# Optimization experiments

Measured on AMD Instinct MI355X. Metric: run time of the kernel, lower is better.

Reference implementation:

```python
import jax, jax.numpy as jnp
import numpy as np

HEAD = 8
EMB = 512
D_K = EMB // HEAD


def setup_inputs() -> dict:
    key = jax.random.key(0)
    ks = jax.random.split(key, 12)
    B, S = 2, 2048
    scale = 1.0 / np.sqrt(EMB)
    inp = {
        "query": jax.random.normal(ks[0], (B, S, EMB), jnp.float32),
        "key": jax.random.normal(ks[1], (B, S, EMB), jnp.float32),
        "value": jax.random.normal(ks[2], (B, S, EMB), jnp.float32),
        # subsequentMask(size): lower-triangular causal mask, shape [1, S, S]
        "mask": jnp.tril(jnp.ones((1, S, S), jnp.int32)),
        "Wq": jax.random.normal(ks[3], (EMB, EMB), jnp.float32) * scale,
        "bq": jnp.zeros((EMB,), jnp.float32),
        "Wk": jax.random.normal(ks[4], (EMB, EMB), jnp.float32) * scale,
        "bk": jnp.zeros((EMB,), jnp.float32),
        "Wv": jax.random.normal(ks[5], (EMB, EMB), jnp.float32) * scale,
        "bv": jnp.zeros((EMB,), jnp.float32),
        "Wo": jax.random.normal(ks[6], (EMB, EMB), jnp.float32) * scale,
        "bo": jnp.zeros((EMB,), jnp.float32),
    }
    return inp


def _split_heads(x, B):
    # [B, S, E] -> [B, H, S, d_k]
    return x.reshape(B, -1, HEAD, D_K).transpose(0, 2, 1, 3)


def reference(query, key, value, mask, Wq, bq, Wk, bk, Wv, bv, Wo, bo):
    B, S, _ = query.shape
    # linear projections (x @ W^T + b, torch nn.Linear convention)
    q = _split_heads(query @ Wq.T + bq, B)
    k = _split_heads(key @ Wk.T + bk, B)
    v = _split_heads(value @ Wv.T + bv, B)
    # scaled dot-product attention; scores [B, H, S, S]
    scores = jnp.einsum('bhqd,bhkd->bhqk', q, k) / jnp.sqrt(jnp.float32(D_K))
    # mask [1,S,S] -> unsqueeze(0) -> [1,1,S,S]; masked_fill(mask==0, -1e9)
    m = mask[None, ...]  # [1, 1, S, S]
    scores = jnp.where(m == 0, jnp.float32(-1e9), scores)
    p_attn = jax.nn.softmax(scores, axis=-1)
    # dropout is identity at inference (deterministic reference)
    x = jnp.einsum('bhqk,bhkd->bhqd', p_attn, v)
    x = x.transpose(0, 2, 1, 3).reshape(B, S, EMB)
    return x @ Wo.T + bo
```

## Files before the change

### kernel.cpp

```cpp
#include <hip/hip_runtime.h>
#include <hip/hip_bf16.h>


#define SEQ 2048
#define EMB 512
#define NH  8
#define DKD 64

typedef __bf16 bf16x8 __attribute__((ext_vector_type(8)));
typedef ushort u16x8  __attribute__((ext_vector_type(8)));
typedef float  f32x4  __attribute__((ext_vector_type(4)));

__device__ __forceinline__ ushort f2bf(float f) {
  unsigned x = __float_as_uint(f);
  return (ushort)((x + 0x7fffu + ((x >> 16) & 1u)) >> 16);
}
__device__ __forceinline__ unsigned pkbf(float a, float b) {
  __hip_bfloat162 h = __float22bfloat162_rn(make_float2(a, b));
  unsigned u;
  __builtin_memcpy(&u, &h, 4);
  return u;
}

__device__ __forceinline__ void cp16(const ushort* g, ushort* l) {
  __builtin_amdgcn_global_load_lds(
      (const __attribute__((address_space(1))) void*)g,
      (__attribute__((address_space(3))) void*)l, 16, 0, 0);
}

__global__ __launch_bounds__(256) void cvt7(
    const float* s0, const float* s1, const float* s2, const float* s3,
    const float* s4, const float* s5, const float* s6,
    ushort* d0, ushort* d1, ushort* d2, ushort* d3,
    ushort* d4, ushort* d5, ushort* d6) {
  const float* src; ushort* dst; int n;
  switch (blockIdx.y) {
    case 0: src = s0; dst = d0; n = 2 * SEQ * EMB; break;
    case 1: src = s1; dst = d1; n = 2 * SEQ * EMB; break;
    case 2: src = s2; dst = d2; n = 2 * SEQ * EMB; break;
    case 3: src = s3; dst = d3; n = EMB * EMB;     break;
    case 4: src = s4; dst = d4; n = EMB * EMB;     break;
    case 5: src = s5; dst = d5; n = EMB * EMB;     break;
    default: src = s6; dst = d6; n = EMB * EMB;    break;
  }
  int i = (blockIdx.x * 256 + threadIdx.x) * 8;
  if (i >= n) return;
  float4 a = *reinterpret_cast<const float4*>(src + i);
  float4 b = *reinterpret_cast<const float4*>(src + i + 4);
  uint4 t = make_uint4(pkbf(a.x, a.y), pkbf(a.z, a.w),
                       pkbf(b.x, b.y), pkbf(b.z, b.w));
  *reinterpret_cast<uint4*>(dst + i) = t;
}

__device__ __forceinline__ void gemm_body(const ushort* __restrict__ X,
                                          const ushort* __restrict__ W,
                                          const float* __restrict__ bias,
                                          void* __restrict__ C,
                                          int mode, bool of32, float oscale,
                                          ushort* sA, ushort* sB) {
  const int N = EMB, K = EMB;
  const int tid = threadIdx.x;
  const int w = tid >> 6, lane = tid & 63, r16 = lane & 15, g = lane >> 4;
  const int nT = N / 64;
  const int m0 = (blockIdx.x / nT) * 128;
  const int n0 = (blockIdx.x % nT) * 64;
  const int wm = w * 32;

  f32x4 acc[2][4] = {};

  auto stage = [&](int buf, int k0) {
#pragma unroll
    for (int i = 0; i < 2; ++i) {
      const int s = i * 256 + w * 64 + lane;
      const int row = s >> 2;
      const int col = (s & 3) ^ ((row >> 1) & 3);
      cp16(X + (size_t)(m0 + row) * K + k0 + col * 8, sA + buf * 4096 + s * 8);
    }
    {
      const int s = w * 64 + lane;
      const int row = s >> 2;
      const int col = (s & 3) ^ ((row >> 1) & 3);
      cp16(W + (size_t)(n0 + row) * K + k0 + col * 8, sB + buf * 2048 + s * 8);
    }
  };

  stage(0, 0);
  const int NIT = K / 32;
  for (int it = 0; it < NIT; ++it) {
    const int cur = it & 1;
    __syncthreads();
    if (it + 1 < NIT) stage(cur ^ 1, (it + 1) * 32);

    const ushort* bA = sA + cur * 4096;
    const ushort* bB = sB + cur * 2048;
    bf16x8 af[2], bfr[4];
#pragma unroll
    for (int f = 0; f < 2; ++f) {
      const int row = wm + f * 16 + r16;
      af[f] = *reinterpret_cast<const bf16x8*>(bA + row * 32 + ((g ^ ((row >> 1) & 3)) << 3));
    }
#pragma unroll
    for (int t = 0; t < 4; ++t) {
      const int row = t * 16 + r16;
      bfr[t] = *reinterpret_cast<const bf16x8*>(bB + row * 32 + ((g ^ ((row >> 1) & 3)) << 3));
    }
#pragma unroll
    for (int f = 0; f < 2; ++f)
#pragma unroll
      for (int t = 0; t < 4; ++t)
        acc[f][t] = __builtin_amdgcn_mfma_f32_16x16x32_bf16(af[f], bfr[t], acc[f][t], 0, 0, 0);
  }

#pragma unroll
  for (int t = 0; t < 4; ++t) {
    const int n = n0 + t * 16 + r16;
    const float bv = bias[n];
#pragma unroll
    for (int f = 0; f < 2; ++f) {
#pragma unroll
      for (int r = 0; r < 4; ++r) {
        const int m = m0 + wm + f * 16 + g * 4 + r;
        const float v = (acc[f][t][r] + bv) * oscale;
        size_t addr;
        if (mode == 0) {
          addr = (size_t)m * N + n;
        } else {
          const int b = m >> 11, s = m & (SEQ - 1);
          const int h = n >> 6, dk = n & (DKD - 1);
          addr = (mode == 1) ? (((size_t)(b * NH + h) * SEQ + s) * DKD + dk)
                             : (((size_t)(b * NH + h) * DKD + dk) * SEQ + s);
        }
        if (of32) ((float*)C)[addr] = v;
        else      ((ushort*)C)[addr] = f2bf(v);
      }
    }
  }
}

__global__ __launch_bounds__(256) void proj_qkv(
    const ushort* Xq, const ushort* Xk, const ushort* Xv,
    const ushort* Wq, const ushort* Wk, const ushort* Wv,
    const float* bq, const float* bk, const float* bv,
    ushort* Qo, ushort* Ko, ushort* Vo) {
  __shared__ __align__(16) ushort sA[2 * 128 * 32];
  __shared__ __align__(16) ushort sB[2 * 64 * 32];
  const int z = blockIdx.z;
  const ushort* X = (z == 0) ? Xq : (z == 1) ? Xk : Xv;
  const ushort* W = (z == 0) ? Wq : (z == 1) ? Wk : Wv;
  const float* bias = (z == 0) ? bq : (z == 1) ? bk : bv;
  ushort* C = (z == 0) ? Qo : (z == 1) ? Ko : Vo;
  gemm_body(X, W, bias, C, (z == 2) ? 2 : 1, false,
            (z == 0) ? 0.18033688011112042f : 1.0f, sA, sB);
}

__global__ __launch_bounds__(256) void out_proj(const ushort* X, const ushort* W,
                                                const float* bias, float* C) {
  __shared__ __align__(16) ushort sA[2 * 128 * 32];
  __shared__ __align__(16) ushort sB[2 * 64 * 32];
  gemm_body(X, W, bias, C, 0, true, 1.0f, sA, sB);
}

__global__ __launch_bounds__(256) void flash_attn(const ushort* __restrict__ Q,
                                                  const ushort* __restrict__ Kb,
                                                  const ushort* __restrict__ Vt,
                                                  ushort* __restrict__ O) {
  __shared__ __align__(16) ushort sK[2][64 * 64];
  __shared__ __align__(16) ushort sV[2][64 * 64];
  __shared__ __align__(16) ushort sP[4][16 * 64];

  const int tid = threadIdx.x, w = tid >> 6, lane = tid & 63;
  const int r16 = lane & 15, g = lane >> 4;
  const int bh = blockIdx.x & 15;
  const int j  = blockIdx.x >> 4;
  const int qb = (j < 16) ? (31 - j) : (j - 16);
  const int q0 = qb * 64 + w * 16;
  const int q  = q0 + r16;

  const ushort* qp = Q + ((size_t)bh * SEQ + q0 + r16) * DKD + g * 8;
  const bf16x8 qf0 = *reinterpret_cast<const bf16x8*>(qp);
  const bf16x8 qf1 = *reinterpret_cast<const bf16x8*>(qp + 32);

  f32x4 oacc[4] = {};
  float psum = 0.f;

  const ushort* kbase = Kb + (size_t)bh * SEQ * DKD;
  const ushort* vbase = Vt + (size_t)bh * DKD * SEQ;

  auto stageKV = [&](int buf, int kb) {
#pragma unroll
    for (int i = 0; i < 2; ++i) {
      const int s = i * 256 + w * 64 + lane;
      const int row = s >> 3;
      const int col = (s & 7) ^ (row & 7);
      cp16(kbase + (size_t)(kb + row) * DKD + col * 8, &sK[buf][(size_t)(i * 256 + w * 64) * 8]);
      cp16(vbase + (size_t)row * SEQ + kb + col * 8,   &sV[buf][(size_t)(i * 256 + w * 64) * 8]);
    }
  };

  stageKV(0, 0);
  const int ntiles = qb + 1;
  for (int kt = 0; kt < ntiles; ++kt) {
    const int cur = kt & 1;
    const int kb = kt * 64;
    __syncthreads();
    if (kt + 1 < ntiles) stageKV(cur ^ 1, (kt + 1) * 64);

    f32x4 sc[4] = {};
#pragma unroll
    for (int t = 0; t < 4; ++t) {
      const int row = t * 16 + r16;
      const bf16x8 a0 = *reinterpret_cast<const bf16x8*>(&sK[cur][row * 64 + (((0 + g) ^ (row & 7)) << 3)]);
      const bf16x8 a1 = *reinterpret_cast<const bf16x8*>(&sK[cur][row * 64 + (((4 + g) ^ (row & 7)) << 3)]);
      sc[t] = __builtin_amdgcn_mfma_f32_16x16x32_bf16(a0, qf0, sc[t], 0, 0, 0);
      sc[t] = __builtin_amdgcn_mfma_f32_16x16x32_bf16(a1, qf1, sc[t], 0, 0, 0);
    }

    const bool diag = (kb + 63) > q0;
    float p[16];
#pragma unroll
    for (int t = 0; t < 4; ++t)
#pragma unroll
      for (int r = 0; r < 4; ++r) {
        float e = __builtin_amdgcn_exp2f(sc[t][r]);
        if (diag && (kb + t * 16 + g * 4 + r) > q) e = 0.f;
        p[t * 4 + r] = e;
      }
    float s0 = (p[0] + p[1]) + (p[2] + p[3]);
    float s1 = (p[4] + p[5]) + (p[6] + p[7]);
    float s2 = (p[8] + p[9]) + (p[10] + p[11]);
    float s3 = (p[12] + p[13]) + (p[14] + p[15]);
    psum += (s0 + s1) + (s2 + s3);

#pragma unroll
    for (int t = 0; t < 4; ++t) {
      const unsigned lo = pkbf(p[t * 4],     p[t * 4 + 1]);
      const unsigned hi = pkbf(p[t * 4 + 2], p[t * 4 + 3]);
      const int key0 = t * 16 + g * 4;
      const int slot = (key0 >> 3) ^ (r16 & 7);
      *reinterpret_cast<uint2*>(&sP[w][r16 * 64 + slot * 8 + (key0 & 7)]) = make_uint2(lo, hi);
    }
    __asm__ volatile("s_waitcnt lgkmcnt(0)" ::: "memory");

    const bf16x8 pf0 = *reinterpret_cast<const bf16x8*>(&sP[w][r16 * 64 + (((0 + g) ^ (r16 & 7)) << 3)]);
    const bf16x8 pf1 = *reinterpret_cast<const bf16x8*>(&sP[w][r16 * 64 + (((4 + g) ^ (r16 & 7)) << 3)]);
#pragma unroll
    for (int t = 0; t < 4; ++t) {
      const int row = t * 16 + r16;
      const bf16x8 b0 = *reinterpret_cast<const bf16x8*>(&sV[cur][row * 64 + (((0 + g) ^ (row & 7)) << 3)]);
      const bf16x8 b1 = *reinterpret_cast<const bf16x8*>(&sV[cur][row * 64 + (((4 + g) ^ (row & 7)) << 3)]);
      oacc[t] = __builtin_amdgcn_mfma_f32_16x16x32_bf16(pf0, b0, oacc[t], 0, 0, 0);
      oacc[t] = __builtin_amdgcn_mfma_f32_16x16x32_bf16(pf1, b1, oacc[t], 0, 0, 0);
    }
  }

  psum += __shfl_xor(psum, 16);
  psum += __shfl_xor(psum, 32);
  const float inv = 1.0f / psum;
  const int b = bh >> 3, h = bh & 7;
#pragma unroll
  for (int r = 0; r < 4; ++r) {
    const float ir = __shfl(inv, g * 4 + r);
    const int mq = q0 + g * 4 + r;
#pragma unroll
    for (int t = 0; t < 4; ++t)
      O[((size_t)b * SEQ + mq) * EMB + h * DKD + t * 16 + r16] = f2bf(oacc[t][r] * ir);
  }
}

extern "C" void kernel_launch(void* const* d_in, const int* in_sizes, int n_in,
                              void* d_out, int out_size, void* d_ws, size_t ws_size,
                              hipStream_t stream) {
  const float* q_in = (const float*)d_in[0];
  const float* k_in = (const float*)d_in[1];
  const float* v_in = (const float*)d_in[2];
  const float* Wq = (const float*)d_in[4];
  const float* bq = (const float*)d_in[5];
  const float* Wk = (const float*)d_in[6];
  const float* bk = (const float*)d_in[7];
  const float* Wv = (const float*)d_in[8];
  const float* bv = (const float*)d_in[9];
  const float* Wo = (const float*)d_in[10];
  const float* bo = (const float*)d_in[11];
  float* out = (float*)d_out;
  ushort* ws = (ushort*)d_ws;

  const size_t NX = (size_t)2 * SEQ * EMB;
  const size_t NW = (size_t)EMB * EMB;
  ushort* Xq = ws;
  ushort* Xk = Xq + NX;
  ushort* Xv = Xk + NX;
  ushort* WqB = Xv + NX;
  ushort* WkB = WqB + NW;
  ushort* WvB = WkB + NW;
  ushort* WoB = WvB + NW;
  ushort* Qb  = WoB + NW;
  ushort* Kbf = Qb + NX;
  ushort* Vbf = Kbf + NX;
  ushort* Ab  = Vbf + NX;

  dim3 blk(256);
  cvt7<<<dim3(1024, 7), blk, 0, stream>>>(q_in, k_in, v_in, Wq, Wk, Wv, Wo,
                                          Xq, Xk, Xv, WqB, WkB, WvB, WoB);
  proj_qkv<<<dim3((2 * SEQ / 128) * (EMB / 64), 1, 3), blk, 0, stream>>>(
      Xq, Xk, Xv, WqB, WkB, WvB, bq, bk, bv, Qb, Kbf, Vbf);
  flash_attn<<<dim3(16 * (SEQ / 64)), blk, 0, stream>>>(Qb, Kbf, Vbf, Ab);
  out_proj<<<dim3((2 * SEQ / 128) * (EMB / 64)), blk, 0, stream>>>(Ab, WoB, bo, out);
}
```

Measured before the change: 174.0 us.

## Split causal attention KV range across two blocks and merge partials

Each query block's KV tiles are split into two halves processed by separate workgroups, doubling the flash attention grid. Each half writes unnormalized fp32 partial outputs and row sums to workspace. A new attn_norm kernel adds the two partials, normalizes, converts to bf16 and writes the head-interleaved layout. This targets causal load imbalance and low block count, at the cost of extra fp32 global traffic and one more launch.

```diff
diff --git a/kernel.cpp b/kernel.cpp
--- a/kernel.cpp
+++ b/kernel.cpp
@@ -163,16 +163,27 @@
 __global__ __launch_bounds__(256) void flash_attn(const ushort* __restrict__ Q,
                                                   const ushort* __restrict__ Kb,
                                                   const ushort* __restrict__ Vt,
-                                                  ushort* __restrict__ O) {
+                                                  float* __restrict__ O0,
+                                                  float* __restrict__ O1,
+                                                  float* __restrict__ P0,
+                                                  float* __restrict__ P1) {
   __shared__ __align__(16) ushort sK[2][64 * 64];
   __shared__ __align__(16) ushort sV[2][64 * 64];
   __shared__ __align__(16) ushort sP[4][16 * 64];
 
   const int tid = threadIdx.x, w = tid >> 6, lane = tid & 63;
   const int r16 = lane & 15, g = lane >> 4;
-  const int bh = blockIdx.x & 15;
-  const int j  = blockIdx.x >> 4;
-  const int qb = (j < 16) ? (31 - j) : (j - 16);
+  const int g2 = blockIdx.x & 3;
+  const int c  = blockIdx.x >> 2;
+  const int bh = c & 15;
+  const int t4 = c >> 4;
+  const int qb = (g2 < 2) ? (31 - t4) : t4;
+  const int half = g2 & 1;
+  const int tiles = qb + 1;
+  const int hs  = (tiles + 1) >> 1;
+  const int kt0 = half ? hs : 0;
+  const int kt1 = half ? tiles : hs;
+
   const int q0 = qb * 64 + w * 16;
   const int q  = q0 + r16;
 
@@ -197,13 +208,12 @@
     }
   };
 
-  stageKV(0, 0);
-  const int ntiles = qb + 1;
-  for (int kt = 0; kt < ntiles; ++kt) {
-    const int cur = kt & 1;
+  if (kt0 < kt1) stageKV(0, kt0 * 64);
+  for (int kt = kt0; kt < kt1; ++kt) {
+    const int cur = (kt - kt0) & 1;
     const int kb = kt * 64;
     __syncthreads();
-    if (kt + 1 < ntiles) stageKV(cur ^ 1, (kt + 1) * 64);
+    if (kt + 1 < kt1) stageKV(cur ^ 1, (kt + 1) * 64);
 
     f32x4 sc[4] = {};
 #pragma unroll
@@ -255,16 +265,40 @@
 
   psum += __shfl_xor(psum, 16);
   psum += __shfl_xor(psum, 32);
-  const float inv = 1.0f / psum;
+  float* Pc = half ? P1 : P0;
+  float* Oc = half ? O1 : O0;
+  if (g == 0) Pc[(size_t)bh * SEQ + q0 + r16] = psum;
+#pragma unroll
+  for (int r = 0; r < 4; ++r) {
+    const int mq = q0 + g * 4 + r;
+#pragma unroll
+    for (int t = 0; t < 4; ++t)
+      Oc[((size_t)bh * SEQ + mq) * DKD + t * 16 + r16] = oacc[t][r];
+  }
+}
+
+__global__ __launch_bounds__(256) void attn_norm(const float* __restrict__ O0,
+                                                 const float* __restrict__ O1,
+                                                 const float* __restrict__ P0,
+                                                 const float* __restrict__ P1,
+                                                 ushort* __restrict__ Ab) {
+  const int idx = blockIdx.x * 256 + threadIdx.x;
+  const int d0 = (idx & 7) * 8;
+  const int s  = (idx >> 3) & (SEQ - 1);
+  const int bh = idx >> 14;
+  const size_t o = ((size_t)bh * SEQ + s) * DKD + d0;
+  const float4 a0 = *reinterpret_cast<const float4*>(O0 + o);
+  const float4 a1 = *reinterpret_cast<const float4*>(O0 + o + 4);
+  const float4 b0 = *reinterpret_cast<const float4*>(O1 + o);
+  const float4 b1 = *reinterpret_cast<const float4*>(O1 + o + 4);
+  const float inv = 1.0f / (P0[(size_t)bh * SEQ + s] + P1[(size_t)bh * SEQ + s]);
+  uint4 t = make_uint4(
+      pkbf((a0.x + b0.x) * inv, (a0.y + b0.y) * inv),
+      pkbf((a0.z + b0.z) * inv, (a0.w + b0.w) * inv),
+      pkbf((a1.x + b1.x) * inv, (a1.y + b1.y) * inv),
+      pkbf((a1.z + b1.z) * inv, (a1.w + b1.w) * inv));
   const int b = bh >> 3, h = bh & 7;
-#pragma unroll
-  for (int r = 0; r < 4; ++r) {
-    const float ir = __shfl(inv, g * 4 + r);
-    const int mq = q0 + g * 4 + r;
-#pragma unroll
-    for (int t = 0; t < 4; ++t)
-      O[((size_t)b * SEQ + mq) * EMB + h * DKD + t * 16 + r16] = f2bf(oacc[t][r] * ir);
-  }
+  *reinterpret_cast<uint4*>(Ab + ((size_t)b * SEQ + s) * EMB + h * DKD + d0) = t;
 }
 
 extern "C" void kernel_launch(void* const* d_in, const int* in_sizes, int n_in,
@@ -297,12 +331,17 @@
   ushort* Kbf = Qb + NX;
   ushort* Vbf = Kbf + NX;
   ushort* Ab  = Vbf + NX;
+  float*  O0  = (float*)(Ab + NX);
+  float*  O1  = O0 + (size_t)2 * NH * SEQ * DKD;
+  float*  P0  = O1 + (size_t)2 * NH * SEQ * DKD;
+  float*  P1  = P0 + (size_t)2 * NH * SEQ;
 
   dim3 blk(256);
   cvt7<<<dim3(1024, 7), blk, 0, stream>>>(q_in, k_in, v_in, Wq, Wk, Wv, Wo,
                                           Xq, Xk, Xv, WqB, WkB, WvB, WoB);
   proj_qkv<<<dim3((2 * SEQ / 128) * (EMB / 64), 1, 3), blk, 0, stream>>>(
       Xq, Xk, Xv, WqB, WkB, WvB, bq, bk, bv, Qb, Kbf, Vbf);
-  flash_attn<<<dim3(16 * (SEQ / 64)), blk, 0, stream>>>(Qb, Kbf, Vbf, Ab);
+  flash_attn<<<dim3(16 * 32 * 2), blk, 0, stream>>>(Qb, Kbf, Vbf, O0, O1, P0, P1);
+  attn_norm<<<dim3(1024), blk, 0, stream>>>(O0, O1, P0, P1, Ab);
   out_proj<<<dim3((2 * SEQ / 128) * (EMB / 64)), blk, 0, stream>>>(Ab, WoB, bo, out);
 }
```

Result: faster. 170.0 us (-2.3%).

## Split attention over key chunks with atomic accumulation and separate normalize kernel

Applied to the files above, without the earlier changes.

Each query block's key range is split into chunks of up to four key tiles, giving 144 work items per head instead of 32. Partial unnormalized outputs and row sums are accumulated with float atomics into a zeroed fp32 buffer, and a new kernel divides and converts to bf16. The goal is better load balance and more blocks for the causal workload. The cost is a memset, many global atomics, an extra kernel launch and extra fp32 memory traffic. It relies on the softmax being computed without a running max (a fixed exp2 with pre-scaled Q), so partial sums can be added directly.

```diff
diff --git a/kernel.cpp b/kernel.cpp
--- a/kernel.cpp
+++ b/kernel.cpp
@@ -163,7 +163,8 @@
 __global__ __launch_bounds__(256) void flash_attn(const ushort* __restrict__ Q,
                                                   const ushort* __restrict__ Kb,
                                                   const ushort* __restrict__ Vt,
-                                                  ushort* __restrict__ O) {
+                                                  float* __restrict__ Oa,
+                                                  float* __restrict__ Pa) {
   __shared__ __align__(16) ushort sK[2][64 * 64];
   __shared__ __align__(16) ushort sV[2][64 * 64];
   __shared__ __align__(16) ushort sP[4][16 * 64];
@@ -171,8 +172,12 @@
   const int tid = threadIdx.x, w = tid >> 6, lane = tid & 63;
   const int r16 = lane & 15, g = lane >> 4;
   const int bh = blockIdx.x & 15;
-  const int j  = blockIdx.x >> 4;
-  const int qb = (j < 16) ? (31 - j) : (j - 16);
+  int rem = blockIdx.x >> 4;
+  int qb = 0;
+  for (;;) { const int cnt = (qb >> 2) + 1; if (rem < cnt) break; rem -= cnt; ++qb; }
+  const int kt0 = rem * 4;
+  const int kt1 = min(kt0 + 4, qb + 1);
+
   const int q0 = qb * 64 + w * 16;
   const int q  = q0 + r16;
 
@@ -197,13 +202,12 @@
     }
   };
 
-  stageKV(0, 0);
-  const int ntiles = qb + 1;
-  for (int kt = 0; kt < ntiles; ++kt) {
-    const int cur = kt & 1;
+  stageKV(0, kt0 * 64);
+  for (int kt = kt0; kt < kt1; ++kt) {
+    const int cur = (kt - kt0) & 1;
     const int kb = kt * 64;
     __syncthreads();
-    if (kt + 1 < ntiles) stageKV(cur ^ 1, (kt + 1) * 64);
+    if (kt + 1 < kt1) stageKV(cur ^ 1, (kt + 1) * 64);
 
     f32x4 sc[4] = {};
 #pragma unroll
@@ -255,16 +259,33 @@
 
   psum += __shfl_xor(psum, 16);
   psum += __shfl_xor(psum, 32);
-  const float inv = 1.0f / psum;
+  if (g == 0) atomicAdd(&Pa[(size_t)bh * SEQ + q0 + r16], psum);
+#pragma unroll
+  for (int r = 0; r < 4; ++r) {
+    const int mq = q0 + g * 4 + r;
+#pragma unroll
+    for (int t = 0; t < 4; ++t)
+      atomicAdd(&Oa[((size_t)bh * SEQ + mq) * DKD + t * 16 + r16], oacc[t][r]);
+  }
+}
+
+__global__ __launch_bounds__(256) void attn_norm(const float* __restrict__ Oa,
+                                                 const float* __restrict__ Pa,
+                                                 ushort* __restrict__ Ab) {
+  const int idx = blockIdx.x * 256 + threadIdx.x;
+  const int d0 = (idx & 7) * 8;
+  const int s  = (idx >> 3) & (SEQ - 1);
+  const int bh = idx >> 14;
+  const size_t o = ((size_t)bh * SEQ + s) * DKD + d0;
+  const float4 a0 = *reinterpret_cast<const float4*>(Oa + o);
+  const float4 a1 = *reinterpret_cast<const float4*>(Oa + o + 4);
+  const float inv = 1.0f / Pa[(size_t)bh * SEQ + s];
+  uint4 t = make_uint4(pkbf(a0.x * inv, a0.y * inv),
+                       pkbf(a0.z * inv, a0.w * inv),
+                       pkbf(a1.x * inv, a1.y * inv),
+                       pkbf(a1.z * inv, a1.w * inv));
   const int b = bh >> 3, h = bh & 7;
-#pragma unroll
-  for (int r = 0; r < 4; ++r) {
-    const float ir = __shfl(inv, g * 4 + r);
-    const int mq = q0 + g * 4 + r;
-#pragma unroll
-    for (int t = 0; t < 4; ++t)
-      O[((size_t)b * SEQ + mq) * EMB + h * DKD + t * 16 + r16] = f2bf(oacc[t][r] * ir);
-  }
+  *reinterpret_cast<uint4*>(Ab + ((size_t)b * SEQ + s) * EMB + h * DKD + d0) = t;
 }
 
 extern "C" void kernel_launch(void* const* d_in, const int* in_sizes, int n_in,
@@ -297,12 +318,17 @@
   ushort* Kbf = Qb + NX;
   ushort* Vbf = Kbf + NX;
   ushort* Ab  = Vbf + NX;
+  float*  Oa  = (float*)(Ab + NX);
+  float*  Pa  = Oa + (size_t)2 * NH * SEQ * DKD;
+  const size_t accBytes = ((size_t)2 * NH * SEQ * DKD + (size_t)2 * NH * SEQ) * 4;
 
   dim3 blk(256);
   cvt7<<<dim3(1024, 7), blk, 0, stream>>>(q_in, k_in, v_in, Wq, Wk, Wv, Wo,
                                           Xq, Xk, Xv, WqB, WkB, WvB, WoB);
   proj_qkv<<<dim3((2 * SEQ / 128) * (EMB / 64), 1, 3), blk, 0, stream>>>(
       Xq, Xk, Xv, WqB, WkB, WvB, bq, bk, bv, Qb, Kbf, Vbf);
-  flash_attn<<<dim3(16 * (SEQ / 64)), blk, 0, stream>>>(Qb, Kbf, Vbf, Ab);
+  hipMemsetAsync(Oa, 0, accBytes, stream);
+  flash_attn<<<dim3(16 * 144), blk, 0, stream>>>(Qb, Kbf, Vbf, Oa, Pa);
+  attn_norm<<<dim3(1024), blk, 0, stream>>>(Oa, Pa, Ab);
   out_proj<<<dim3((2 * SEQ / 128) * (EMB / 64)), blk, 0, stream>>>(Ab, WoB, bo, out);
 }
```

Result: slower. 177.6 us (+2.1%).
